# Optimization experiments

Hardware: AMD Instinct MI355X
Metric: run time of the kernel (lower is better)

Reference implementation:

```python
import jax, jax.numpy as jnp
import numpy as np

HEADS = 8
HC = 64  # num_head_channels
DIM = 256
HIDDEN = HEADS * HC
EPS = 1e-5


def setup_inputs() -> dict:
    key = jax.random.key(0)
    ks = jax.random.split(key, 6)
    x = jax.random.normal(ks[0], (16, DIM, 64, 64), dtype=jnp.float32)
    Wq = jax.random.normal(ks[1], (HIDDEN, DIM), dtype=jnp.float32) * 0.02
    Wk = jax.random.normal(ks[2], (HIDDEN, DIM), dtype=jnp.float32) * 0.02
    Wv = jax.random.normal(ks[3], (HIDDEN, DIM), dtype=jnp.float32) * 0.02
    Wo = jax.random.normal(ks[4], (DIM, HIDDEN), dtype=jnp.float32) * 0.02
    bo = jnp.zeros((DIM,), dtype=jnp.float32)
    gamma = jnp.ones((DIM,), dtype=jnp.float32)
    beta = jnp.zeros((DIM,), dtype=jnp.float32)
    return {"x": x, "Wq": Wq, "Wk": Wk, "Wv": Wv, "Wo": Wo, "bo": bo,
            "gamma": gamma, "beta": beta}


def reference(x, Wq, Wk, Wv, Wo, bo, gamma, beta):
    b, c, h, w = x.shape
    n = h * w
    scale = HC ** (-0.5)
    xf = x.reshape(b, c, n)  # [b, c, n]
    # 1x1 convs == channel matmuls
    q = jnp.einsum('oc,bcn->bon', Wq, xf).reshape(b * HEADS, HC, n)
    k = jnp.einsum('oc,bcn->bon', Wk, xf).reshape(b * HEADS, HC, n)
    v = jnp.einsum('oc,bcn->bon', Wv, xf).reshape(b * HEADS, HC, n)
    q = jax.nn.softmax(q, axis=1) * scale      # softmax over head channels
    k = jax.nn.softmax(k, axis=2)              # softmax over spatial
    # context = k @ v^T : [bh, hc, hc]
    context = jnp.einsum('bdn,ben->bde', k, v)
    # output = context^T @ q : [bh, hc, n]
    out = jnp.einsum('bde,bdn->ben', context, q)
    out = out.reshape(b, HIDDEN, n)
    # to_out conv1x1 + bias
    y = jnp.einsum('oc,bcn->bon', Wo, out) + bo[None, :, None]
    # GroupNorm(num_groups=1): normalize over (c, n) per sample
    mean = jnp.mean(y, axis=(1, 2), keepdims=True)
    var = jnp.var(y, axis=(1, 2), keepdims=True)
    y = (y - mean) * jax.lax.rsqrt(var + EPS)
    y = y * gamma[None, :, None] + beta[None, :, None]
    return y.reshape(b, c, h, w) + x
```

## Files before the change

kernel.cpp:

```cpp
#include <hip/hip_runtime.h>
#include <hip/hip_bf16.h>

#define DEV __device__ __forceinline__

constexpr int B_ = 16, CDIM = 256, NDIM = 4096, HID = 512, HEADS = 8, HC = 64;
constexpr float EPSV = 1e-5f;

using bf16x8 = __attribute__((ext_vector_type(8))) __bf16;
using f32x4  = __attribute__((ext_vector_type(4))) float;
using s16x8  = __attribute__((ext_vector_type(8))) short;
using s16x4  = __attribute__((ext_vector_type(4))) short;

DEV short f2bf(float f) {
  __hip_bfloat16 h = __float2bfloat16(f);
  return *reinterpret_cast<short*>(&h);
}
DEV f32x4 MFMA(bf16x8 a, bf16x8 b, f32x4 c) {
  return __builtin_amdgcn_mfma_f32_16x16x32_bf16(a, b, c, 0, 0, 0);
}

__global__ void wconv_kernel(const float* __restrict__ Wq, const float* __restrict__ Wk,
                             const float* __restrict__ Wv, const float* __restrict__ Wo,
                             short* __restrict__ Wall, short* __restrict__ Wo_b) {
  const int i = blockIdx.x * 256 + threadIdx.x;
  const int nw = HID * CDIM;
  if (i < nw) Wall[i] = f2bf(Wq[i]);
  else if (i < 2 * nw) Wall[i] = f2bf(Wk[i - nw]);
  else if (i < 3 * nw) Wall[i] = f2bf(Wv[i - 2 * nw]);
  if (i < CDIM * HID) Wo_b[i] = f2bf(Wo[i]);
}

__global__ __launch_bounds__(256) void xconv_kernel(const float* __restrict__ x, short* __restrict__ xt) {
  __shared__ float t[32][33];
  const int bi = blockIdx.z, n0 = blockIdx.x * 32, c0 = blockIdx.y * 32;
  const int tx = threadIdx.x, ty = threadIdx.y;
  const float* xb = x + (size_t)bi * CDIM * NDIM;
#pragma unroll
  for (int i = 0; i < 32; i += 8)
    t[ty + i][tx] = xb[(size_t)(c0 + ty + i) * NDIM + n0 + tx];
  __syncthreads();
  short* xtb = xt + (size_t)bi * NDIM * CDIM;
#pragma unroll
  for (int i = 0; i < 32; i += 8)
    xtb[(size_t)(n0 + ty + i) * CDIM + c0 + tx] = f2bf(t[tx][ty + i]);
}

DEV bf16x8 xs_read(const char* xs, int row, int colShorts) {
  int byte = (row << 9) + (colShorts << 1);
  byte ^= (row & 7) << 4;
  return *(const bf16x8*)(xs + byte);
}

__global__ __launch_bounds__(256) void kvslice_kernel(const short* __restrict__ Wall,
                                                      const short* __restrict__ xt,
                                                      float* __restrict__ ctxp,
                                                      float* __restrict__ statp,
                                                      int nper) {
  const int bh = blockIdx.x, sl = blockIdx.y, nsl = gridDim.y;
  const int bi = bh >> 3, h = bh & 7;
  const int tid = threadIdx.x, lane = tid & 63, wid = tid >> 6;
  const int ro = lane & 15, g = lane >> 4, ko = g * 8;
  const short* Wk = Wall + (size_t)(HID + h * HC) * CDIM;
  const short* Wv = Wall + (size_t)(2 * HID + h * HC) * CDIM;
  const char* xbase = (const char*)(xt + ((size_t)bi * NDIM + (size_t)sl * nper) * CDIM);

  __shared__ __align__(16) char xs[64 * 512];
  __shared__ short pl[64][68];
  __shared__ short vl[64][68];

  bf16x8 ak[8], av[8];
#pragma unroll
  for (int ks = 0; ks < 8; ++ks) {
    ak[ks] = *(const bf16x8*)&Wk[(size_t)(wid * 16 + ro) * CDIM + ks * 32 + ko];
    av[ks] = *(const bf16x8*)&Wv[(size_t)(wid * 16 + ro) * CDIM + ks * 32 + ko];
  }
  float sacc[4] = {0.f, 0.f, 0.f, 0.f};
  f32x4 cacc[4] = {};
  const int drow = wid * 16 + g * 4;

  s16x8 r[8];
#pragma unroll
  for (int it = 0; it < 8; ++it) r[it] = *(const s16x8*)(xbase + it * 4096 + tid * 16);

  for (int nc = 0; nc < nper; nc += 64) {
    if (nc > 0) {
#pragma unroll
      for (int ks = 0; ks < 2; ++ks) {
        bf16x8 pa = *(const bf16x8*)&pl[wid * 16 + ro][ks * 32 + ko];
#pragma unroll
        for (int et = 0; et < 4; ++et) {
          bf16x8 vb = *(const bf16x8*)&vl[et * 16 + ro][ks * 32 + ko];
          cacc[et] = MFMA(pa, vb, cacc[et]);
        }
      }
    }
#pragma unroll
    for (int it = 0; it < 8; ++it) {
      const int fb = it * 4096 + tid * 16;
      *(s16x8*)(xs + (fb ^ (((fb >> 9) & 7) << 4))) = r[it];
    }
    __syncthreads();
    if (nc + 64 < nper) {
      const char* srcn = xbase + (size_t)(nc + 64) * 512;
#pragma unroll
      for (int it = 0; it < 8; ++it) r[it] = *(const s16x8*)(srcn + it * 4096 + tid * 16);
    }
    f32x4 kacc[4] = {};
    f32x4 vacc[4] = {};
#pragma unroll
    for (int ks = 0; ks < 8; ++ks)
#pragma unroll
      for (int nt = 0; nt < 4; ++nt) {
        bf16x8 bfr = xs_read(xs, nt * 16 + ro, ks * 32 + ko);
        kacc[nt] = MFMA(ak[ks], bfr, kacc[nt]);
        vacc[nt] = MFMA(av[ks], bfr, vacc[nt]);
      }
#pragma unroll
    for (int nt = 0; nt < 4; ++nt)
#pragma unroll
      for (int j = 0; j < 4; ++j) {
        const float p = __expf(kacc[nt][j]);
        sacc[j] += p;
        pl[drow + j][nt * 16 + ro] = f2bf(p);
        vl[drow + j][nt * 16 + ro] = f2bf(vacc[nt][j]);
      }
    __syncthreads();
  }
#pragma unroll
  for (int ks = 0; ks < 2; ++ks) {
    bf16x8 pa = *(const bf16x8*)&pl[wid * 16 + ro][ks * 32 + ko];
#pragma unroll
    for (int et = 0; et < 4; ++et) {
      bf16x8 vb = *(const bf16x8*)&vl[et * 16 + ro][ks * 32 + ko];
      cacc[et] = MFMA(pa, vb, cacc[et]);
    }
  }
#pragma unroll
  for (int o = 1; o < 16; o <<= 1)
#pragma unroll
    for (int j = 0; j < 4; ++j) sacc[j] += __shfl_xor(sacc[j], o);

  float* cp = ctxp + ((size_t)bh * nsl + sl) * HC * HC;
#pragma unroll
  for (int et = 0; et < 4; ++et)
#pragma unroll
    for (int j = 0; j < 4; ++j)
      cp[(drow + j) * HC + et * 16 + ro] = cacc[et][j];
  if (ro == 0) {
    float* sp = statp + ((size_t)bh * nsl + sl) * HC;
#pragma unroll
    for (int j = 0; j < 4; ++j) sp[drow + j] = sacc[j];
  }
}

__global__ __launch_bounds__(256) void ctxred_kernel(const float* __restrict__ ctxp,
                                                     const float* __restrict__ statp,
                                                     short* __restrict__ ctx, int nsl) {
  const int bh = blockIdx.x, tid = threadIdx.x;
  const int d = tid >> 2, e0 = (tid & 3) * 16;
  const float* sp = statp + (size_t)bh * nsl * HC;
  float stot = 0.f;
  for (int i = 0; i < nsl; ++i) stot += sp[i * HC + d];
  const float inv = 1.f / stot;
  const float* cp = ctxp + (size_t)bh * nsl * HC * HC;
  short* cb = ctx + (size_t)bh * HC * HC;
  for (int e = e0; e < e0 + 16; ++e) {
    float u = 0.f;
    for (int i = 0; i < nsl; ++i) u += cp[i * HC * HC + d * HC + e];
    cb[d * HC + e] = f2bf(u * inv);
  }
}

__global__ __launch_bounds__(256) void meff_kernel(const short* __restrict__ Wo_b,
                                                   const short* __restrict__ ctx,
                                                   short* __restrict__ Meff) {
  const int bh = blockIdx.x, bi = bh >> 3, h = bh & 7;
  const int tid = threadIdx.x, lane = tid & 63, wid = tid >> 6;
  const int ro = lane & 15, ko = (lane >> 4) * 8;
  const short* Arow = Wo_b + h * HC;
  const short* Bc = ctx + (size_t)bh * HC * HC;
  f32x4 acc[4][4] = {};
#pragma unroll
  for (int ks = 0; ks < 64; ks += 32) {
    bf16x8 af[4], bv[4];
#pragma unroll
    for (int mi = 0; mi < 4; ++mi)
      af[mi] = *(const bf16x8*)&Arow[(size_t)(wid * 64 + mi * 16 + ro) * HID + ks + ko];
#pragma unroll
    for (int ni = 0; ni < 4; ++ni)
      bv[ni] = *(const bf16x8*)&Bc[(ni * 16 + ro) * HC + ks + ko];
#pragma unroll
    for (int mi = 0; mi < 4; ++mi)
#pragma unroll
      for (int ni = 0; ni < 4; ++ni) acc[mi][ni] = MFMA(af[mi], bv[ni], acc[mi][ni]);
  }
  short* Mb = Meff + (size_t)bi * CDIM * HID + h * HC;
  const int r0 = wid * 64 + ((lane >> 4) << 2), c0 = lane & 15;
#pragma unroll
  for (int mi = 0; mi < 4; ++mi)
#pragma unroll
    for (int ni = 0; ni < 4; ++ni)
#pragma unroll
      for (int j = 0; j < 4; ++j)
        Mb[(size_t)(r0 + mi * 16 + j) * HID + ni * 16 + c0] = f2bf(acc[mi][ni][j]);
}

__global__ __launch_bounds__(256) void qsm_kernel(const short* __restrict__ Wall,
                                                  const short* __restrict__ xt,
                                                  short* __restrict__ qtc,
                                                  int NC, int nbase) {
  const int bi = blockIdx.y, n0 = blockIdx.x * 64;
  const int tid = threadIdx.x, lane = tid & 63, wid = tid >> 6;
  const int rl = lane & 15, g = lane >> 4;
  __shared__ short xs[64][264];
  const short* xb = xt + ((size_t)bi * NDIM + nbase + n0) * CDIM;
  const int srow = tid >> 2, scol = (tid & 3) * 64;
#pragma unroll
  for (int i = 0; i < 8; ++i)
    *(s16x8*)&xs[srow][scol + i * 8] = *(const s16x8*)&xb[(size_t)srow * CDIM + scol + i * 8];
  __syncthreads();
#pragma unroll 1
  for (int hp = 0; hp < 2; ++hp) {
    const int h = wid * 2 + hp;
    const short* Wq = Wall + (size_t)h * HC * CDIM;
    f32x4 acc[4][4] = {};
#pragma unroll
    for (int ks = 0; ks < 8; ++ks) {
      bf16x8 bfr[4];
#pragma unroll
      for (int nt = 0; nt < 4; ++nt) bfr[nt] = *(const bf16x8*)&xs[nt * 16 + rl][ks * 32 + g * 8];
#pragma unroll
      for (int rt = 0; rt < 4; ++rt) {
        bf16x8 af = *(const bf16x8*)&Wq[(size_t)(rt * 16 + rl) * CDIM + ks * 32 + g * 8];
#pragma unroll
        for (int nt = 0; nt < 4; ++nt) acc[rt][nt] = MFMA(af, bfr[nt], acc[rt][nt]);
      }
    }
    float mx[4];
#pragma unroll
    for (int nt = 0; nt < 4; ++nt) {
      float v = acc[0][nt][0];
#pragma unroll
      for (int rt = 0; rt < 4; ++rt)
#pragma unroll
        for (int j = 0; j < 4; ++j) v = fmaxf(v, acc[rt][nt][j]);
      mx[nt] = v;
    }
#pragma unroll
    for (int nt = 0; nt < 4; ++nt) {
      mx[nt] = fmaxf(mx[nt], __shfl_xor(mx[nt], 16));
      mx[nt] = fmaxf(mx[nt], __shfl_xor(mx[nt], 32));
    }
    float sm[4] = {0.f, 0.f, 0.f, 0.f};
#pragma unroll
    for (int rt = 0; rt < 4; ++rt)
#pragma unroll
      for (int nt = 0; nt < 4; ++nt)
#pragma unroll
        for (int j = 0; j < 4; ++j) {
          const float e = __expf(acc[rt][nt][j] - mx[nt]);
          acc[rt][nt][j] = e;
          sm[nt] += e;
        }
#pragma unroll
    for (int nt = 0; nt < 4; ++nt) {
      sm[nt] += __shfl_xor(sm[nt], 16);
      sm[nt] += __shfl_xor(sm[nt], 32);
      sm[nt] = 0.125f / sm[nt];
    }
#pragma unroll
    for (int nt = 0; nt < 4; ++nt) {
      short* qr = qtc + ((size_t)bi * NC + n0 + nt * 16 + rl) * HID + h * HC + g * 4;
#pragma unroll
      for (int rt = 0; rt < 4; ++rt) {
        s16x4 v;
#pragma unroll
        for (int j = 0; j < 4; ++j) v[j] = f2bf(acc[rt][nt][j] * sm[nt]);
        *(s16x4*)&qr[rt * 16] = v;
      }
    }
  }
}

__global__ __launch_bounds__(256) void ymm_kernel(const short* __restrict__ Meff,
                                                  const short* __restrict__ qtc,
                                                  const float* __restrict__ bo,
                                                  float* __restrict__ out,
                                                  float2* __restrict__ partials,
                                                  int NC, int nbase, int pbase) {
  constexpr int K = HID, LDT = 72;
  __shared__ short Al[128 * LDT];
  __shared__ short Bl[128 * LDT];
  __shared__ float a1[4], a2[4];
  const int bi = blockIdx.z, mt = blockIdx.y, nt = blockIdx.x;
  const int tid = threadIdx.x, lane = tid & 63, wid = tid >> 6;
  const int wr = (wid >> 1) * 64, wc = (wid & 1) * 64;
  const short* Ab = Meff + (size_t)bi * CDIM * HID + (size_t)mt * 128 * K;
  const short* Bb = qtc + ((size_t)bi * NC + (size_t)nt * 128) * K;
  f32x4 acc[4][4] = {};
  const int sr = tid >> 3, sk = (tid & 7) * 8;
  const int ro = lane & 15, ko = (lane >> 4) * 8;
  for (int kt = 0; kt < K; kt += 64) {
#pragma unroll
    for (int i = 0; i < 4; ++i) {
      const int r = sr + 32 * i;
      *(s16x8*)&Al[r * LDT + sk] = *(const s16x8*)&Ab[(size_t)r * K + kt + sk];
      *(s16x8*)&Bl[r * LDT + sk] = *(const s16x8*)&Bb[(size_t)r * K + kt + sk];
    }
    __syncthreads();
#pragma unroll
    for (int ks = 0; ks < 64; ks += 32) {
      bf16x8 af[4], bfr[4];
#pragma unroll
      for (int i = 0; i < 4; ++i) {
        af[i]  = *(const bf16x8*)&Al[(wr + i * 16 + ro) * LDT + ks + ko];
        bfr[i] = *(const bf16x8*)&Bl[(wc + i * 16 + ro) * LDT + ks + ko];
      }
#pragma unroll
      for (int mi = 0; mi < 4; ++mi)
#pragma unroll
        for (int ni = 0; ni < 4; ++ni)
          acc[mi][ni] = MFMA(af[mi], bfr[ni], acc[mi][ni]);
    }
    __syncthreads();
  }
  const int r0 = mt * 128 + wr + ((lane >> 4) << 2);
  const int c0 = nbase + nt * 128 + wc + ro;
  float* C = out + (size_t)bi * CDIM * NDIM;
  float s1 = 0.f, s2 = 0.f;
#pragma unroll
  for (int mi = 0; mi < 4; ++mi)
#pragma unroll
    for (int j = 0; j < 4; ++j) {
      const int row = r0 + mi * 16 + j;
      const float b = bo[row];
#pragma unroll
      for (int ni = 0; ni < 4; ++ni) {
        const float v = acc[mi][ni][j] + b;
        C[(size_t)row * NDIM + c0 + ni * 16] = v;
        s1 += v;
        s2 += v * v;
      }
    }
#pragma unroll
  for (int o = 1; o < 64; o <<= 1) { s1 += __shfl_xor(s1, o); s2 += __shfl_xor(s2, o); }
  if (lane == 0) { a1[wid] = s1; a2[wid] = s2; }
  __syncthreads();
  if (tid == 0)
    partials[bi * 64 + pbase + mt * gridDim.x + nt] =
        make_float2(a1[0] + a1[1] + a1[2] + a1[3], a2[0] + a2[1] + a2[2] + a2[3]);
}

__global__ void redstats_kernel(const float2* __restrict__ partials, float* __restrict__ stats) {
  const int bi = blockIdx.x, l = threadIdx.x;
  float2 p = partials[bi * 64 + l];
  float s1 = p.x, s2 = p.y;
#pragma unroll
  for (int o = 32; o; o >>= 1) { s1 += __shfl_xor(s1, o); s2 += __shfl_xor(s2, o); }
  if (l == 0) { stats[bi * 2] = s1; stats[bi * 2 + 1] = s2; }
}

__global__ __launch_bounds__(256) void final_kernel(float* __restrict__ y, const float* __restrict__ x,
                                                    const float* __restrict__ gamma, const float* __restrict__ beta,
                                                    const float* __restrict__ stats) {
  const int bi = blockIdx.y;
  constexpr float invN = 1.f / ((float)CDIM * NDIM);
  const float mean = stats[bi * 2] * invN;
  const float var = stats[bi * 2 + 1] * invN - mean * mean;
  const float rstd = rsqrtf(var + EPSV);
  float4* y4 = (float4*)(y + (size_t)bi * CDIM * NDIM);
  const float4* x4 = (const float4*)(x + (size_t)bi * CDIM * NDIM);
  for (int i = blockIdx.x * 256 + threadIdx.x; i < CDIM * NDIM / 4; i += 128 * 256) {
    const int c = i >> 10;
    const float g = gamma[c] * rstd;
    const float b = beta[c] - mean * g;
    float4 v = y4[i];
    const float4 xv = x4[i];
    v.x = v.x * g + b + xv.x;
    v.y = v.y * g + b + xv.y;
    v.z = v.z * g + b + xv.z;
    v.w = v.w * g + b + xv.w;
    y4[i] = v;
  }
}

extern "C" void kernel_launch(void* const* d_in, const int* in_sizes, int n_in,
                              void* d_out, int out_size, void* d_ws, size_t ws_size,
                              hipStream_t stream) {
  const float* x     = (const float*)d_in[0];
  const float* Wq    = (const float*)d_in[1];
  const float* Wk    = (const float*)d_in[2];
  const float* Wv    = (const float*)d_in[3];
  const float* Wo    = (const float*)d_in[4];
  const float* bo    = (const float*)d_in[5];
  const float* gamma = (const float*)d_in[6];
  const float* beta  = (const float*)d_in[7];
  float* out = (float*)d_out;

  char* w = (char*)d_ws;
  size_t off = 0;
  auto alloc = [&](size_t n) {
    char* p = w + off;
    off = (off + n + 255) & ~(size_t)255;
    return p;
  };
  constexpr int NSL = 8;
  short* xt    = (short*)alloc((size_t)B_ * NDIM * CDIM * 2);
  short* Wall  = (short*)alloc((size_t)3 * HID * CDIM * 2);
  short* Wo_b  = (short*)alloc((size_t)CDIM * HID * 2);
  short* ctx   = (short*)alloc((size_t)128 * HC * HC * 2);
  short* Meff  = (short*)alloc((size_t)B_ * CDIM * HID * 2);
  float2* partials = (float2*)alloc((size_t)B_ * 64 * sizeof(float2));
  float* stats = (float*)alloc(32 * 4);
  float* ctxp  = (float*)alloc((size_t)128 * NSL * HC * HC * 4);
  float* statp = (float*)alloc((size_t)128 * NSL * HC * 4);
  const size_t base = off;

  int NC = 4096;
  while (NC > 64 && base + (size_t)B_ * NC * HID * 2 > ws_size) NC >>= 1;
  short* qtc = (short*)alloc((size_t)B_ * NC * HID * 2);

  wconv_kernel<<<1536, 256, 0, stream>>>(Wq, Wk, Wv, Wo, Wall, Wo_b);
  xconv_kernel<<<dim3(128, 8, B_), dim3(32, 8), 0, stream>>>(x, xt);
  kvslice_kernel<<<dim3(128, NSL), 256, 0, stream>>>(Wall, xt, ctxp, statp, NDIM / NSL);
  ctxred_kernel<<<128, 256, 0, stream>>>(ctxp, statp, ctx, NSL);
  meff_kernel<<<128, 256, 0, stream>>>(Wo_b, ctx, Meff);
  const int nchunks = NDIM / NC;
  for (int c = 0; c < nchunks; ++c) {
    qsm_kernel<<<dim3(NC / 64, B_), 256, 0, stream>>>(Wall, xt, qtc, NC, c * NC);
    ymm_kernel<<<dim3(NC / 128, 2, B_), 256, 0, stream>>>(Meff, qtc, bo, out, partials,
                                                          NC, c * NC, c * 2 * (NC / 128));
  }
  redstats_kernel<<<B_, 64, 0, stream>>>(partials, stats);
  final_kernel<<<dim3(128, B_), 256, 0, stream>>>(out, x, gamma, beta, stats);
}
```

Before: 230.4 us.

## Split q-softmax heads across waves with LDS reduction and swizzled x tile

Restructures the q projection and softmax kernel so each of the four waves computes 16 channels of every head, looping over all 8 heads. The per-position softmax sums are combined across waves through shared memory. The x tile is stored in an XOR-swizzled shared layout to cut bank conflicts, and the next head's weight fragments are prefetched into registers. The max subtraction is dropped from the softmax, which risks overflow for large logits, and the change adds a block barrier for every head.

```diff
diff --git a/kernel.cpp b/kernel.cpp
--- a/kernel.cpp
+++ b/kernel.cpp
@@ -211,74 +211,69 @@
                                                   int NC, int nbase) {
   const int bi = blockIdx.y, n0 = blockIdx.x * 64;
   const int tid = threadIdx.x, lane = tid & 63, wid = tid >> 6;
-  const int rl = lane & 15, g = lane >> 4;
-  __shared__ short xs[64][264];
-  const short* xb = xt + ((size_t)bi * NDIM + nbase + n0) * CDIM;
-  const int srow = tid >> 2, scol = (tid & 3) * 64;
-#pragma unroll
-  for (int i = 0; i < 8; ++i)
-    *(s16x8*)&xs[srow][scol + i * 8] = *(const s16x8*)&xb[(size_t)srow * CDIM + scol + i * 8];
+  const int ro = lane & 15, g = lane >> 4, ko = g * 8;
+  __shared__ __align__(16) char xs[64 * 512];
+  __shared__ float ps[8 * 4 * 4 * 16];
+  const char* xbase = (const char*)(xt + ((size_t)bi * NDIM + nbase + n0) * CDIM);
+#pragma unroll
+  for (int it = 0; it < 8; ++it) {
+    const int fb = it * 4096 + tid * 16;
+    *(s16x8*)(xs + (fb ^ (((fb >> 9) & 7) << 4))) = *(const s16x8*)(xbase + fb);
+  }
   __syncthreads();
+
+  const short* wbase = Wall + (size_t)(wid * 16 + ro) * CDIM + ko;
+  bf16x8 aq[8], aqn[8];
+#pragma unroll
+  for (int ks = 0; ks < 8; ++ks) aq[ks] = *(const bf16x8*)(wbase + ks * 32);
+
 #pragma unroll 1
-  for (int hp = 0; hp < 2; ++hp) {
-    const int h = wid * 2 + hp;
-    const short* Wq = Wall + (size_t)h * HC * CDIM;
-    f32x4 acc[4][4] = {};
-#pragma unroll
-    for (int ks = 0; ks < 8; ++ks) {
-      bf16x8 bfr[4];
-#pragma unroll
-      for (int nt = 0; nt < 4; ++nt) bfr[nt] = *(const bf16x8*)&xs[nt * 16 + rl][ks * 32 + g * 8];
-#pragma unroll
-      for (int rt = 0; rt < 4; ++rt) {
-        bf16x8 af = *(const bf16x8*)&Wq[(size_t)(rt * 16 + rl) * CDIM + ks * 32 + g * 8];
-#pragma unroll
-        for (int nt = 0; nt < 4; ++nt) acc[rt][nt] = MFMA(af, bfr[nt], acc[rt][nt]);
-      }
-    }
-    float mx[4];
+  for (int h = 0; h < HEADS; ++h) {
+    if (h < 7) {
+      const short* wn = wbase + (size_t)(h + 1) * HC * CDIM;
+#pragma unroll
+      for (int ks = 0; ks < 8; ++ks) aqn[ks] = *(const bf16x8*)(wn + ks * 32);
+    }
+    f32x4 kacc[4] = {};
+#pragma unroll
+    for (int ks = 0; ks < 8; ++ks)
+#pragma unroll
+      for (int nt = 0; nt < 4; ++nt)
+        kacc[nt] = MFMA(aq[ks], xs_read(xs, nt * 16 + ro, ks * 32 + ko), kacc[nt]);
+    float tsum[4];
 #pragma unroll
     for (int nt = 0; nt < 4; ++nt) {
-      float v = acc[0][nt][0];
-#pragma unroll
-      for (int rt = 0; rt < 4; ++rt)
-#pragma unroll
-        for (int j = 0; j < 4; ++j) v = fmaxf(v, acc[rt][nt][j]);
-      mx[nt] = v;
+#pragma unroll
+      for (int j = 0; j < 4; ++j) kacc[nt][j] = __expf(kacc[nt][j]);
+      tsum[nt] = kacc[nt][0] + kacc[nt][1] + kacc[nt][2] + kacc[nt][3];
     }
 #pragma unroll
     for (int nt = 0; nt < 4; ++nt) {
-      mx[nt] = fmaxf(mx[nt], __shfl_xor(mx[nt], 16));
-      mx[nt] = fmaxf(mx[nt], __shfl_xor(mx[nt], 32));
-    }
-    float sm[4] = {0.f, 0.f, 0.f, 0.f};
-#pragma unroll
-    for (int rt = 0; rt < 4; ++rt)
-#pragma unroll
-      for (int nt = 0; nt < 4; ++nt)
-#pragma unroll
-        for (int j = 0; j < 4; ++j) {
-          const float e = __expf(acc[rt][nt][j] - mx[nt]);
-          acc[rt][nt][j] = e;
-          sm[nt] += e;
-        }
+      tsum[nt] += __shfl_xor(tsum[nt], 16);
+      tsum[nt] += __shfl_xor(tsum[nt], 32);
+    }
+    if (g == 0) {
+#pragma unroll
+      for (int nt = 0; nt < 4; ++nt) ps[((h * 4 + wid) * 4 + nt) * 16 + ro] = tsum[nt];
+    }
+    __syncthreads();
+    float inv[4];
 #pragma unroll
     for (int nt = 0; nt < 4; ++nt) {
-      sm[nt] += __shfl_xor(sm[nt], 16);
-      sm[nt] += __shfl_xor(sm[nt], 32);
-      sm[nt] = 0.125f / sm[nt];
-    }
+      const float t = ps[((h * 4 + 0) * 4 + nt) * 16 + ro] + ps[((h * 4 + 1) * 4 + nt) * 16 + ro] +
+                      ps[((h * 4 + 2) * 4 + nt) * 16 + ro] + ps[((h * 4 + 3) * 4 + nt) * 16 + ro];
+      inv[nt] = 0.125f / t;
+    }
+    short* qh = qtc + ((size_t)bi * NC + n0) * HID + h * HC + wid * 16 + g * 4;
 #pragma unroll
     for (int nt = 0; nt < 4; ++nt) {
-      short* qr = qtc + ((size_t)bi * NC + n0 + nt * 16 + rl) * HID + h * HC + g * 4;
-#pragma unroll
-      for (int rt = 0; rt < 4; ++rt) {
-        s16x4 v;
-#pragma unroll
-        for (int j = 0; j < 4; ++j) v[j] = f2bf(acc[rt][nt][j] * sm[nt]);
-        *(s16x4*)&qr[rt * 16] = v;
-      }
-    }
+      s16x4 v;
+#pragma unroll
+      for (int j = 0; j < 4; ++j) v[j] = f2bf(kacc[nt][j] * inv[nt]);
+      *(s16x4*)(qh + (size_t)(nt * 16 + ro) * HID) = v;
+    }
+#pragma unroll
+    for (int ks = 0; ks < 8; ++ks) aq[ks] = aqn[ks];
   }
 }
 
```

Result: faster. 220.3 us (-4.4%).
